# Optimization experiments

Hardware: AMD Instinct MI355X
Metric: run time of the kernel (lower is better)

The kernel has to match this reference:

```python
import jax, jax.numpy as jnp
import numpy as np

N_NODES = 100000
N_EDGES = 1600000
IN_DIM = 128
HID = 128


def setup_inputs() -> dict:
    key = jax.random.key(0)
    ks = jax.random.split(key, 8)
    x = jax.random.normal(ks[0], (N_NODES, IN_DIM), dtype=jnp.float32)
    edge_index = jax.random.randint(ks[1], (2, N_EDGES), 0, N_NODES, dtype=jnp.int32)
    s = 1.0 / np.sqrt(IN_DIM)
    # layer 1: in_dim -> hidden; layer 2: hidden -> hidden
    Wl1 = jax.random.uniform(ks[2], (IN_DIM, HID), jnp.float32, -s, s)
    bl1 = jnp.zeros((HID,), jnp.float32)
    Wr1 = jax.random.uniform(ks[3], (IN_DIM, HID), jnp.float32, -s, s)
    s2 = 1.0 / np.sqrt(HID)
    Wl2 = jax.random.uniform(ks[4], (HID, HID), jnp.float32, -s2, s2)
    bl2 = jnp.zeros((HID,), jnp.float32)
    Wr2 = jax.random.uniform(ks[5], (HID, HID), jnp.float32, -s2, s2)
    return {"x": x, "edge_index": edge_index, "Wl1": Wl1, "bl1": bl1, "Wr1": Wr1,
            "Wl2": Wl2, "bl2": bl2, "Wr2": Wr2}


def _sage_conv(h, src, dst, Wl, bl, Wr, n_nodes):
    # mean aggregation of neighbor (source) features at destination nodes
    msg = h[src]                                               # [E, D] gather
    agg = jax.ops.segment_sum(msg, dst, num_segments=n_nodes)  # [N, D]
    deg = jax.ops.segment_sum(jnp.ones((src.shape[0],), h.dtype), dst,
                              num_segments=n_nodes)            # [N]
    agg = agg / jnp.maximum(deg, 1.0)[:, None]
    # PyG SAGEConv: lin_l(aggregated) + lin_r(root); lin_r has no bias
    return agg @ Wl + bl + h @ Wr


def reference(x, edge_index, Wl1, bl1, Wr1, Wl2, bl2, Wr2):
    src, dst = edge_index[0], edge_index[1]
    n = x.shape[0]
    h = jax.nn.relu(_sage_conv(x, src, dst, Wl1, bl1, Wr1, n))
    # dropout is identity in eval mode
    h = jax.nn.relu(_sage_conv(h, src, dst, Wl2, bl2, Wr2, n))
    return h
```

## Files before the change

### kernel.cpp

```cpp
#include <hip/hip_runtime.h>
#include <stdint.h>

#define DIM 128

typedef __attribute__((ext_vector_type(8))) short short8;
typedef __attribute__((ext_vector_type(4))) float floatx4;

__device__ __forceinline__ unsigned short f2bf(float f){
  union { float f; unsigned int i; } c; c.f = f;
  unsigned int u = c.i;
  return (unsigned short)((u + 0x7fffu + ((u >> 16) & 1u)) >> 16);
}
__device__ __forceinline__ float up_lo(unsigned int v){ return __uint_as_float(v << 16); }
__device__ __forceinline__ float up_hi(unsigned int v){ return __uint_as_float(v & 0xffff0000u); }


__global__ __launch_bounds__(256) void k_cast(const float* __restrict__ in,
    unsigned short* __restrict__ out, int n4){
  int i = blockIdx.x * 256 + threadIdx.x;
  int stride = gridDim.x * 256;
  for (; i < n4; i += stride){
    float4 v = ((const float4*)in)[i];
    ushort4 o;
    o.x = f2bf(v.x); o.y = f2bf(v.y); o.z = f2bf(v.z); o.w = f2bf(v.w);
    ((ushort4*)out)[i] = o;
  }
}


__global__ __launch_bounds__(256) void k_hist256(const int* __restrict__ dst, int E,
    int* __restrict__ bktCnt){
  __shared__ int h[256];
  h[threadIdx.x] = 0;
  __syncthreads();
  int i = blockIdx.x * 256 + threadIdx.x;
  int stride = gridDim.x * 256;
  for (; i < E; i += stride) atomicAdd(&h[dst[i] >> 9], 1);
  __syncthreads();
  int v = h[threadIdx.x];
  if (v) atomicAdd(&bktCnt[threadIdx.x], v);
}

__global__ __launch_bounds__(256) void k_scanB(const int* __restrict__ bktCnt,
    int* __restrict__ bktBase, int NB){
  __shared__ int sd[256];
  int t = threadIdx.x;
  int v = (t < NB) ? bktCnt[t] : 0;
  sd[t] = v;
  __syncthreads();
  #pragma unroll
  for (int off = 1; off < 256; off <<= 1){
    int x = (t >= off) ? sd[t - off] : 0;
    __syncthreads();
    sd[t] += x;
    __syncthreads();
  }
  bktBase[t] = sd[t] - v;
}


__global__ __launch_bounds__(256) void k_hist(const int* __restrict__ dst, int E,
                                              int* __restrict__ deg){
  int e = blockIdx.x * 256 + threadIdx.x;
  if (e < E) atomicAdd(&deg[dst[e]], 1);
}

__global__ __launch_bounds__(256) void k_scan1(const int* __restrict__ deg, int N,
    int* __restrict__ out, int* __restrict__ bsum){
  __shared__ int sd[256];
  int t = threadIdx.x;
  int base = blockIdx.x * 1024 + t * 4;
  int v0=0, v1=0, v2=0, v3=0;
  if (base + 3 < N) { int4 q = *(const int4*)(deg + base); v0=q.x; v1=q.y; v2=q.z; v3=q.w; }
  else {
    if (base + 0 < N) v0 = deg[base + 0];
    if (base + 1 < N) v1 = deg[base + 1];
    if (base + 2 < N) v2 = deg[base + 2];
  }
  int s = v0 + v1 + v2 + v3;
  sd[t] = s;
  __syncthreads();
  #pragma unroll
  for (int off = 1; off < 256; off <<= 1){
    int x = (t >= off) ? sd[t - off] : 0;
    __syncthreads();
    sd[t] += x;
    __syncthreads();
  }
  int inc = sd[t];
  int exc = inc - s;
  if (base + 0 < N) out[base + 0] = exc;
  if (base + 1 < N) out[base + 1] = exc + v0;
  if (base + 2 < N) out[base + 2] = exc + v0 + v1;
  if (base + 3 < N) out[base + 3] = exc + v0 + v1 + v2;
  if (t == 255) bsum[blockIdx.x] = inc;
}

__global__ __launch_bounds__(128) void k_scan2(int* __restrict__ bsum, int nb){
  __shared__ int sd[128];
  int t = threadIdx.x;
  int v = (t < nb) ? bsum[t] : 0;
  sd[t] = v;
  __syncthreads();
  #pragma unroll
  for (int off = 1; off < 128; off <<= 1){
    int x = (t >= off) ? sd[t - off] : 0;
    __syncthreads();
    sd[t] += x;
    __syncthreads();
  }
  if (t < nb) bsum[t] = sd[t] - v;
}

__global__ __launch_bounds__(256) void k_scan3(int* __restrict__ rowptr,
    const int* __restrict__ bsum, int N, int E, int* __restrict__ cursor){
  int i = blockIdx.x * 256 + threadIdx.x;
  if (i < N){
    int v = rowptr[i] + bsum[i >> 10];
    rowptr[i] = v;
    cursor[i] = v;
  }
  if (i == 0) rowptr[N] = E;
}

__global__ __launch_bounds__(256) void k_fill(const int* __restrict__ src,
    const int* __restrict__ dst, int E, int* __restrict__ cursor, int* __restrict__ col){
  int e = blockIdx.x * 256 + threadIdx.x;
  if (e < E){
    int d = dst[e];
    int pos = atomicAdd(&cursor[d], 1);
    col[pos] = src[e];
  }
}


__global__ __launch_bounds__(256) void k_bin(const int* __restrict__ src,
    const int* __restrict__ dst, int E,
    const int* __restrict__ bucketBase, int* __restrict__ cursor,
    int2* __restrict__ binned, int NB){
  __shared__ int2 buf[4096];
  __shared__ unsigned char bidArr[4096];
  __shared__ int cnt[256], startA[256], gstart[256], gbase[256];
  int t = threadIdx.x;
  cnt[t] = 0;
  if (t < NB) gbase[t] = bucketBase[t];
  __syncthreads();
  int base = blockIdx.x * 4096;
  int s_[16], d_[16], r_[16];
  #pragma unroll
  for (int i = 0; i < 16; ++i){
    int e = base + i * 256 + t;
    bool v = (e < E);
    s_[i] = v ? src[e] : 0;
    d_[i] = v ? dst[e] : -1;
    r_[i] = v ? atomicAdd(&cnt[d_[i] >> 9], 1) : 0;
  }
  __syncthreads();
  int v = cnt[t];
  startA[t] = v;
  __syncthreads();
  #pragma unroll
  for (int off = 1; off < 256; off <<= 1){
    int y = (t >= off) ? startA[t - off] : 0;
    __syncthreads();
    startA[t] += y;
    __syncthreads();
  }
  int incl = startA[t];
  __syncthreads();
  startA[t] = incl - v;
  __syncthreads();
  #pragma unroll
  for (int i = 0; i < 16; ++i){
    if (d_[i] >= 0){
      int b = d_[i] >> 9;
      int slot = startA[b] + r_[i];
      buf[slot] = make_int2(s_[i], d_[i]);
      bidArr[slot] = (unsigned char)b;
    }
  }
  if (cnt[t] > 0) gstart[t] = atomicAdd(&cursor[t], cnt[t]);
  __syncthreads();
  int total = startA[255] + cnt[255];
  for (int j = t; j < total; j += 256){
    int b = bidArr[j];
    binned[gbase[b] + gstart[b] + (j - startA[b])] = buf[j];
  }
}


__global__ __launch_bounds__(256) void k_csr2(const int2* __restrict__ binned,
    const int* __restrict__ bktBase, int N, int* __restrict__ rowptr,
    int* __restrict__ col){
  __shared__ int cnt[512], excl[512], cur[512];
  __shared__ int sd[256];
  int b = blockIdx.x;
  int node0 = b << 9;
  int nNodes = min(512, N - node0);
  int t = threadIdx.x;
  cnt[t] = 0; cnt[t + 256] = 0;
  __syncthreads();
  int lo = bktBase[b], hi = bktBase[b + 1];
  for (int e = lo + t; e < hi; e += 256)
    atomicAdd(&cnt[binned[e].y - node0], 1);
  __syncthreads();
  int c0 = cnt[2 * t], c1 = cnt[2 * t + 1];
  int ps = c0 + c1;
  sd[t] = ps;
  __syncthreads();
  #pragma unroll
  for (int off = 1; off < 256; off <<= 1){
    int x = (t >= off) ? sd[t - off] : 0;
    __syncthreads();
    sd[t] += x;
    __syncthreads();
  }
  int pexcl = sd[t] - ps;
  excl[2 * t] = pexcl;
  excl[2 * t + 1] = pexcl + c0;
  cur[2 * t] = 0; cur[2 * t + 1] = 0;
  __syncthreads();
  for (int j = t; j < nNodes; j += 256) rowptr[node0 + j] = lo + excl[j];
  if (t == 0) rowptr[node0 + nNodes] = hi;
  for (int e = lo + t; e < hi; e += 256){
    int2 pr = binned[e];
    int dl = pr.y - node0;
    int loc = atomicAdd(&cur[dl], 1);
    col[lo + excl[dl] + loc] = pr.x;
  }
}


__device__ __forceinline__ void acc8(float* a, uint4 u){
  a[0] += up_lo(u.x); a[1] += up_hi(u.x);
  a[2] += up_lo(u.y); a[3] += up_hi(u.y);
  a[4] += up_lo(u.z); a[5] += up_hi(u.z);
  a[6] += up_lo(u.w); a[7] += up_hi(u.w);
}

__global__ __launch_bounds__(256) void k_agg_bf(const unsigned short* __restrict__ feat,
    const int* __restrict__ rowptr, const int* __restrict__ col,
    unsigned short* __restrict__ out, int N){
  int wid = (blockIdx.x * 256 + threadIdx.x) >> 6;
  if (wid >= N) return;
  int lane = threadIdx.x & 63;
  int q = lane >> 4, s = lane & 15;
  int beg = rowptr[wid], end = rowptr[wid + 1];
  int deg = end - beg;
  float a[8];
  #pragma unroll
  for (int i = 0; i < 8; ++i) a[i] = 0.f;

  int myIdx = (beg + lane < end) ? col[beg + lane] : 0;

  int o0 = q, o1 = 4 + q, o2 = 8 + q, o3 = 12 + q;
  int n0 = __shfl(myIdx, o0, 64);
  int n1 = __shfl(myIdx, o1, 64);
  int n2 = __shfl(myIdx, o2, 64);
  int n3 = __shfl(myIdx, o3, 64);
  uint4 u0 = ((const uint4*)(feat + (size_t)n0 * DIM))[s];
  uint4 u1 = ((const uint4*)(feat + (size_t)n1 * DIM))[s];
  uint4 u2 = ((const uint4*)(feat + (size_t)n2 * DIM))[s];
  uint4 u3 = ((const uint4*)(feat + (size_t)n3 * DIM))[s];

  bool g1 = deg > 16;
  int o4 = 16 + q, o5 = 20 + q, o6 = 24 + q, o7 = 28 + q;
  uint4 u4, u5, u6, u7;
  if (g1){
    int n4 = __shfl(myIdx, o4, 64);
    int n5 = __shfl(myIdx, o5, 64);
    int n6 = __shfl(myIdx, o6, 64);
    int n7 = __shfl(myIdx, o7, 64);
    u4 = ((const uint4*)(feat + (size_t)n4 * DIM))[s];
    u5 = ((const uint4*)(feat + (size_t)n5 * DIM))[s];
    u6 = ((const uint4*)(feat + (size_t)n6 * DIM))[s];
    u7 = ((const uint4*)(feat + (size_t)n7 * DIM))[s];
  }

  if (o0 < deg) acc8(a, u0);
  if (o1 < deg) acc8(a, u1);
  if (o2 < deg) acc8(a, u2);
  if (o3 < deg) acc8(a, u3);
  if (g1){
    if (o4 < deg) acc8(a, u4);
    if (o5 < deg) acc8(a, u5);
    if (o6 < deg) acc8(a, u6);
    if (o7 < deg) acc8(a, u7);
  }

  for (int e = beg + 32; e < end; e += 16){
    int i0 = e + q, i1 = e + 4 + q, i2 = e + 8 + q, i3 = e + 12 + q;
    int m0 = col[i0 < end ? i0 : beg];
    int m1 = col[i1 < end ? i1 : beg];
    int m2 = col[i2 < end ? i2 : beg];
    int m3 = col[i3 < end ? i3 : beg];
    uint4 v0 = ((const uint4*)(feat + (size_t)m0 * DIM))[s];
    uint4 v1 = ((const uint4*)(feat + (size_t)m1 * DIM))[s];
    uint4 v2 = ((const uint4*)(feat + (size_t)m2 * DIM))[s];
    uint4 v3 = ((const uint4*)(feat + (size_t)m3 * DIM))[s];
    if (i0 < end) acc8(a, v0);
    if (i1 < end) acc8(a, v1);
    if (i2 < end) acc8(a, v2);
    if (i3 < end) acc8(a, v3);
  }

  #pragma unroll
  for (int i = 0; i < 8; ++i){
    a[i] += __shfl_xor(a[i], 16, 64);
    a[i] += __shfl_xor(a[i], 32, 64);
  }
  if (q == 0){
    int d = deg;
    float r = 1.0f / (float)(d > 1 ? d : 1);
    uint4 o;
    o.x = (unsigned int)f2bf(a[0] * r) | ((unsigned int)f2bf(a[1] * r) << 16);
    o.y = (unsigned int)f2bf(a[2] * r) | ((unsigned int)f2bf(a[3] * r) << 16);
    o.z = (unsigned int)f2bf(a[4] * r) | ((unsigned int)f2bf(a[5] * r) << 16);
    o.w = (unsigned int)f2bf(a[6] * r) | ((unsigned int)f2bf(a[7] * r) << 16);
    ((uint4*)(out + (size_t)wid * DIM))[s] = o;
  }
}


__global__ __launch_bounds__(256) void k_agg_f32(const float* __restrict__ feat,
    const int* __restrict__ rowptr, const int* __restrict__ col,
    unsigned short* __restrict__ out, int N){
  int wid = (blockIdx.x * 256 + threadIdx.x) >> 6;
  if (wid >= N) return;
  int lane = threadIdx.x & 63;
  int beg = rowptr[wid], end = rowptr[wid + 1];
  float a0 = 0.f, a1 = 0.f;
  int off = lane * 2;
  int e = beg;
  for (; e + 4 <= end; e += 4){
    int s0 = col[e], s1 = col[e+1], s2 = col[e+2], s3 = col[e+3];
    float2 v0 = *(const float2*)(feat + (size_t)s0 * DIM + off);
    float2 v1 = *(const float2*)(feat + (size_t)s1 * DIM + off);
    float2 v2 = *(const float2*)(feat + (size_t)s2 * DIM + off);
    float2 v3 = *(const float2*)(feat + (size_t)s3 * DIM + off);
    a0 += v0.x + v1.x + v2.x + v3.x;
    a1 += v0.y + v1.y + v2.y + v3.y;
  }
  for (; e < end; ++e){
    float2 v = *(const float2*)(feat + (size_t)col[e] * DIM + off);
    a0 += v.x; a1 += v.y;
  }
  int d = end - beg;
  float r = 1.0f / (float)(d > 1 ? d : 1);
  a0 *= r; a1 *= r;
  unsigned int o = (unsigned int)f2bf(a0) | ((unsigned int)f2bf(a1) << 16);
  *(unsigned int*)(out + (size_t)wid * DIM + off) = o;
}


template<bool OUTBF>
__global__ __launch_bounds__(256) void k_gemm_r(const unsigned short* __restrict__ A1,
    const unsigned short* __restrict__ A2,
    const float* __restrict__ Wl, const float* __restrict__ Wr,
    const float* __restrict__ bias,
    float* __restrict__ outf, unsigned short* __restrict__ outb, int M)
{
  int lane = threadIdx.x & 63;
  int c = lane & 15, quad = lane >> 4;
  int gwid = blockIdx.x * 4 + (threadIdx.x >> 6);
  int nwaves = gridDim.x * 4;
  int half = gwid & 1;
  int colbase = half * 64;

  short8 B[2][4][4];
  #pragma unroll
  for (int w = 0; w < 2; ++w){
    const float* W = w ? Wr : Wl;
    #pragma unroll
    for (int km = 0; km < 4; ++km){
      #pragma unroll
      for (int j = 0; j < 4; ++j){
        union { short8 v; unsigned short u[8]; } tb;
        #pragma unroll
        for (int i = 0; i < 8; ++i)
          tb.u[i] = f2bf(W[(km * 32 + quad * 8 + i) * 128 + colbase + j * 16 + c]);
        B[w][km][j] = tb.v;
      }
    }
  }
  float bv[4];
  #pragma unroll
  for (int j = 0; j < 4; ++j) bv[j] = bias[colbase + j * 16 + c];

  int ntasks = M >> 4;
  for (int task = gwid >> 1; task < ntasks; task += nwaves >> 1){
    int row0 = task << 4;
    const unsigned short* ap1 = A1 + (size_t)(row0 + c) * DIM + quad * 8;
    const unsigned short* ap2 = A2 + (size_t)(row0 + c) * DIM + quad * 8;
    short8 a1[4], a2[4];
    #pragma unroll
    for (int km = 0; km < 4; ++km){
      a1[km] = *(const short8*)(ap1 + km * 32);
      a2[km] = *(const short8*)(ap2 + km * 32);
    }
    floatx4 acc[4];
    #pragma unroll
    for (int j = 0; j < 4; ++j) acc[j] = (floatx4){0.f, 0.f, 0.f, 0.f};
    #pragma unroll
    for (int km = 0; km < 4; ++km){
      #pragma unroll
      for (int j = 0; j < 4; ++j){
        acc[j] = __builtin_amdgcn_mfma_f32_16x16x32_bf16(a1[km], B[0][km][j], acc[j], 0, 0, 0);
        acc[j] = __builtin_amdgcn_mfma_f32_16x16x32_bf16(a2[km], B[1][km][j], acc[j], 0, 0, 0);
      }
    }
    #pragma unroll
    for (int j = 0; j < 4; ++j){
      int colIdx = colbase + j * 16 + c;
      #pragma unroll
      for (int r = 0; r < 4; ++r){
        int row = row0 + quad * 4 + r;
        float v = fmaxf(acc[j][r] + bv[j], 0.f);
        if (OUTBF) outb[(size_t)row * DIM + colIdx] = f2bf(v);
        else       outf[(size_t)row * DIM + colIdx] = v;
      }
    }
  }
}


__global__ __launch_bounds__(256) void k_gemm_f(const unsigned short* __restrict__ A1,
    const float* __restrict__ A2f,
    const float* __restrict__ Wl, const float* __restrict__ Wr,
    const float* __restrict__ bias, float* __restrict__ outf, int M)
{
  __shared__ unsigned short lds[2 * 128 * 128];
  for (int h = threadIdx.x; h < 128 * 128; h += 256){
    int k = h >> 7, n = h & 127;
    int idx = n * 128 + ((((k >> 3) ^ (n & 7)) << 3)) + (k & 7);
    lds[idx]         = f2bf(Wl[h]);
    lds[16384 + idx] = f2bf(Wr[h]);
  }
  __syncthreads();
  int lane = threadIdx.x & 63;
  int c = lane & 15, quad = lane >> 4;
  int gwid = blockIdx.x * 4 + (threadIdx.x >> 6);
  int nwaves = gridDim.x * 4;
  int ntasks = M >> 4;
  for (int task = gwid; task < ntasks; task += nwaves){
    int row0 = task << 4;
    floatx4 acc[8];
    #pragma unroll
    for (int j = 0; j < 8; ++j) acc[j] = (floatx4){0.f, 0.f, 0.f, 0.f};
    const unsigned short* ap1 = A1 + (size_t)(row0 + c) * DIM + quad * 8;
    #pragma unroll
    for (int km = 0; km < 4; ++km){
      short8 a = *(const short8*)(ap1 + km * 32);
      int kb = (km << 2) + quad;
      #pragma unroll
      for (int j = 0; j < 8; ++j){
        short8 b = *(const short8*)(&lds[(j * 16 + c) * 128 + ((kb ^ (c & 7)) << 3)]);
        acc[j] = __builtin_amdgcn_mfma_f32_16x16x32_bf16(a, b, acc[j], 0, 0, 0);
      }
    }
    #pragma unroll
    for (int km = 0; km < 4; ++km){
      const float* ap2 = A2f + (size_t)(row0 + c) * DIM + quad * 8;
      float4 p0 = *(const float4*)(ap2 + km * 32);
      float4 p1 = *(const float4*)(ap2 + km * 32 + 4);
      union { short8 v; unsigned short u[8]; } ua;
      ua.u[0] = f2bf(p0.x); ua.u[1] = f2bf(p0.y);
      ua.u[2] = f2bf(p0.z); ua.u[3] = f2bf(p0.w);
      ua.u[4] = f2bf(p1.x); ua.u[5] = f2bf(p1.y);
      ua.u[6] = f2bf(p1.z); ua.u[7] = f2bf(p1.w);
      int kb = (km << 2) + quad;
      #pragma unroll
      for (int j = 0; j < 8; ++j){
        short8 b = *(const short8*)(&lds[16384 + (j * 16 + c) * 128 + ((kb ^ (c & 7)) << 3)]);
        acc[j] = __builtin_amdgcn_mfma_f32_16x16x32_bf16(ua.v, b, acc[j], 0, 0, 0);
      }
    }
    #pragma unroll
    for (int j = 0; j < 8; ++j){
      int colIdx = j * 16 + c;
      float bvv = bias[colIdx];
      #pragma unroll
      for (int r = 0; r < 4; ++r){
        int row = row0 + quad * 4 + r;
        outf[(size_t)row * DIM + colIdx] = fmaxf(acc[j][r] + bvv, 0.f);
      }
    }
  }
}


extern "C" void kernel_launch(void* const* d_in, const int* in_sizes, int n_in,
                              void* d_out, int out_size, void* d_ws, size_t ws_size,
                              hipStream_t stream)
{
  const float* x   = (const float*)d_in[0];
  const int*   ei  = (const int*)d_in[1];
  const float* Wl1 = (const float*)d_in[2];
  const float* bl1 = (const float*)d_in[3];
  const float* Wr1 = (const float*)d_in[4];
  const float* Wl2 = (const float*)d_in[5];
  const float* bl2 = (const float*)d_in[6];
  const float* Wr2 = (const float*)d_in[7];

  const int N = in_sizes[0] / DIM;
  const int E = in_sizes[1] / 2;
  const int* src  = ei;
  const int* dstI = ei + E;
  const int NB = (N + 511) >> 9;

  char* p = (char*)d_ws;
  auto alloc = [&](size_t bytes) -> char* {
    char* r = p; p += (bytes + 255) & ~((size_t)255); return r;
  };
  int* rowptr   = (int*)alloc((size_t)(N + 1) * 4);
  int* deg      = (int*)alloc((size_t)N * 4);
  int* bsum     = (int*)alloc(1024);
  int* bktCnt   = (int*)alloc(1024);
  int* bktBase  = (int*)alloc(2048);
  int* bktCur   = (int*)alloc(1024);
  int* col      = (int*)alloc((size_t)E * 4);
  unsigned short* aggb = (unsigned short*)alloc((size_t)N * DIM * 2);
  unsigned short* xb   = (unsigned short*)alloc((size_t)N * DIM * 2);
  unsigned short* h1b  = (unsigned short*)alloc((size_t)N * DIM * 2);
  size_t need_big = (size_t)(p - (char*)d_ws);
  const bool big = (ws_size >= need_big) && (NB <= 255);
  int2* binned = (int2*)aggb;

  int gE = (E + 255) / 256;
  int gAgg = (N * 64 + 255) / 256;

  if (big){
    hipMemsetAsync(bktCnt, 0, 1024, stream);
    hipMemsetAsync(bktCur, 0, 1024, stream);
    k_hist256<<<1024, 256, 0, stream>>>(dstI, E, bktCnt);
    k_scanB<<<1, 256, 0, stream>>>(bktCnt, bktBase, NB);
    k_bin<<<(E + 4095) / 4096, 256, 0, stream>>>(src, dstI, E, bktBase, bktCur,
                                                 binned, NB);
    k_csr2<<<NB, 256, 0, stream>>>(binned, bktBase, N, rowptr, col);
    int n4 = N * DIM / 4;
    k_cast<<<8192, 256, 0, stream>>>(x, xb, n4);
    k_agg_bf<<<gAgg, 256, 0, stream>>>(xb, rowptr, col, aggb, N);
    k_gemm_r<true><<<512, 256, 0, stream>>>(aggb, xb, Wl1, Wr1, bl1,
                                            nullptr, h1b, N);
    k_agg_bf<<<gAgg, 256, 0, stream>>>(h1b, rowptr, col, aggb, N);
    k_gemm_r<false><<<512, 256, 0, stream>>>(aggb, h1b, Wl2, Wr2, bl2,
                                             (float*)d_out, nullptr, N);
  } else {
    hipMemsetAsync(deg, 0, (size_t)N * 4, stream);
    k_hist<<<gE, 256, 0, stream>>>(dstI, E, deg);
    int nb = (N + 1023) / 1024;
    k_scan1<<<nb, 256, 0, stream>>>(deg, N, rowptr, bsum);
    k_scan2<<<1, 128, 0, stream>>>(bsum, nb);
    k_scan3<<<(N + 255) / 256, 256, 0, stream>>>(rowptr, bsum, N, E, deg);
    k_fill<<<gE, 256, 0, stream>>>(src, dstI, E, deg, col);
    float* h1 = (float*)d_out;
    k_agg_f32<<<gAgg, 256, 0, stream>>>(x, rowptr, col, aggb, N);
    k_gemm_f<<<512, 256, 0, stream>>>(aggb, x, Wl1, Wr1, bl1, h1, N);
    k_agg_f32<<<gAgg, 256, 0, stream>>>(h1, rowptr, col, aggb, N);
    k_gemm_f<<<512, 256, 0, stream>>>(aggb, h1, Wl2, Wr2, bl2, (float*)d_out, N);
  }
}
```

Baseline: 338.4 us.

## Fuse cast with bucket histogram, prefetch GEMM tiles, widen CSR build blocks

Merges the fp32-to-bf16 cast of x with the destination bucket histogram into one kernel and merges the two memsets into one by making the counter buffers adjacent. The binning chunk shrinks to 2048 edges per block, the CSR build runs 1024 threads per bucket, and the GEMM now software-prefetches the next task's A tiles while computing the current one, with launch bounds raised for occupancy. The aim is to cut launch overhead and latency stalls. The cost is more registers from the prefetch and fewer blocks for the cast.

Measured after the change: 329.4 us. 2.7% less time.

```diff
diff --git a/kernel.cpp b/kernel.cpp
--- a/kernel.cpp
+++ b/kernel.cpp
@@ -15,27 +15,21 @@
 __device__ __forceinline__ float up_hi(unsigned int v){ return __uint_as_float(v & 0xffff0000u); }
 
 
-__global__ __launch_bounds__(256) void k_cast(const float* __restrict__ in,
-    unsigned short* __restrict__ out, int n4){
+__global__ __launch_bounds__(256) void k_prep(const float* __restrict__ in,
+    unsigned short* __restrict__ out, int n4,
+    const int* __restrict__ dst, int E, int* __restrict__ bktCnt){
+  __shared__ int h[256];
+  h[threadIdx.x] = 0;
+  __syncthreads();
   int i = blockIdx.x * 256 + threadIdx.x;
   int stride = gridDim.x * 256;
-  for (; i < n4; i += stride){
-    float4 v = ((const float4*)in)[i];
+  for (int k = i; k < n4; k += stride){
+    float4 v = ((const float4*)in)[k];
     ushort4 o;
     o.x = f2bf(v.x); o.y = f2bf(v.y); o.z = f2bf(v.z); o.w = f2bf(v.w);
-    ((ushort4*)out)[i] = o;
-  }
-}
-
-
-__global__ __launch_bounds__(256) void k_hist256(const int* __restrict__ dst, int E,
-    int* __restrict__ bktCnt){
-  __shared__ int h[256];
-  h[threadIdx.x] = 0;
-  __syncthreads();
-  int i = blockIdx.x * 256 + threadIdx.x;
-  int stride = gridDim.x * 256;
-  for (; i < E; i += stride) atomicAdd(&h[dst[i] >> 9], 1);
+    ((ushort4*)out)[k] = o;
+  }
+  for (int k = i; k < E; k += stride) atomicAdd(&h[dst[k] >> 9], 1);
   __syncthreads();
   int v = h[threadIdx.x];
   if (v) atomicAdd(&bktCnt[threadIdx.x], v);
@@ -134,21 +128,23 @@
 }
 
 
+#define BINCH 2048
+
 __global__ __launch_bounds__(256) void k_bin(const int* __restrict__ src,
     const int* __restrict__ dst, int E,
     const int* __restrict__ bucketBase, int* __restrict__ cursor,
     int2* __restrict__ binned, int NB){
-  __shared__ int2 buf[4096];
-  __shared__ unsigned char bidArr[4096];
+  __shared__ int2 buf[BINCH];
+  __shared__ unsigned char bidArr[BINCH];
   __shared__ int cnt[256], startA[256], gstart[256], gbase[256];
   int t = threadIdx.x;
   cnt[t] = 0;
   if (t < NB) gbase[t] = bucketBase[t];
   __syncthreads();
-  int base = blockIdx.x * 4096;
-  int s_[16], d_[16], r_[16];
-  #pragma unroll
-  for (int i = 0; i < 16; ++i){
+  int base = blockIdx.x * BINCH;
+  int s_[8], d_[8], r_[8];
+  #pragma unroll
+  for (int i = 0; i < 8; ++i){
     int e = base + i * 256 + t;
     bool v = (e < E);
     s_[i] = v ? src[e] : 0;
@@ -171,7 +167,7 @@
   startA[t] = incl - v;
   __syncthreads();
   #pragma unroll
-  for (int i = 0; i < 16; ++i){
+  for (int i = 0; i < 8; ++i){
     if (d_[i] >= 0){
       int b = d_[i] >> 9;
       int slot = startA[b] + r_[i];
@@ -189,7 +185,7 @@
 }
 
 
-__global__ __launch_bounds__(256) void k_csr2(const int2* __restrict__ binned,
+__global__ __launch_bounds__(1024) void k_csr2(const int2* __restrict__ binned,
     const int* __restrict__ bktBase, int N, int* __restrict__ rowptr,
     int* __restrict__ col){
   __shared__ int cnt[512], excl[512], cur[512];
@@ -198,31 +194,36 @@
   int node0 = b << 9;
   int nNodes = min(512, N - node0);
   int t = threadIdx.x;
-  cnt[t] = 0; cnt[t + 256] = 0;
+  if (t < 512){ cnt[t] = 0; cur[t] = 0; }
   __syncthreads();
   int lo = bktBase[b], hi = bktBase[b + 1];
-  for (int e = lo + t; e < hi; e += 256)
+  for (int e = lo + t; e < hi; e += 1024)
     atomicAdd(&cnt[binned[e].y - node0], 1);
   __syncthreads();
-  int c0 = cnt[2 * t], c1 = cnt[2 * t + 1];
-  int ps = c0 + c1;
-  sd[t] = ps;
+  int c0 = 0, c1 = 0, ps = 0;
+  if (t < 256){
+    c0 = cnt[2 * t]; c1 = cnt[2 * t + 1];
+    ps = c0 + c1;
+    sd[t] = ps;
+  }
   __syncthreads();
   #pragma unroll
   for (int off = 1; off < 256; off <<= 1){
-    int x = (t >= off) ? sd[t - off] : 0;
-    __syncthreads();
-    sd[t] += x;
-    __syncthreads();
-  }
-  int pexcl = sd[t] - ps;
-  excl[2 * t] = pexcl;
-  excl[2 * t + 1] = pexcl + c0;
-  cur[2 * t] = 0; cur[2 * t + 1] = 0;
-  __syncthreads();
-  for (int j = t; j < nNodes; j += 256) rowptr[node0 + j] = lo + excl[j];
+    int x = 0;
+    if (t < 256 && t >= off) x = sd[t - off];
+    __syncthreads();
+    if (t < 256) sd[t] += x;
+    __syncthreads();
+  }
+  if (t < 256){
+    int pexcl = sd[t] - ps;
+    excl[2 * t] = pexcl;
+    excl[2 * t + 1] = pexcl + c0;
+  }
+  __syncthreads();
+  for (int j = t; j < nNodes; j += 1024) rowptr[node0 + j] = lo + excl[j];
   if (t == 0) rowptr[node0 + nNodes] = hi;
-  for (int e = lo + t; e < hi; e += 256){
+  for (int e = lo + t; e < hi; e += 1024){
     int2 pr = binned[e];
     int dl = pr.y - node0;
     int loc = atomicAdd(&cur[dl], 1);
@@ -354,7 +355,7 @@
 
 
 template<bool OUTBF>
-__global__ __launch_bounds__(256) void k_gemm_r(const unsigned short* __restrict__ A1,
+__global__ __launch_bounds__(256, 2) void k_gemm_r(const unsigned short* __restrict__ A1,
     const unsigned short* __restrict__ A2,
     const float* __restrict__ Wl, const float* __restrict__ Wr,
     const float* __restrict__ bias,
@@ -388,15 +389,28 @@
   for (int j = 0; j < 4; ++j) bv[j] = bias[colbase + j * 16 + c];
 
   int ntasks = M >> 4;
-  for (int task = gwid >> 1; task < ntasks; task += nwaves >> 1){
-    int row0 = task << 4;
-    const unsigned short* ap1 = A1 + (size_t)(row0 + c) * DIM + quad * 8;
-    const unsigned short* ap2 = A2 + (size_t)(row0 + c) * DIM + quad * 8;
-    short8 a1[4], a2[4];
+  int stride = nwaves >> 1;
+  int task = gwid >> 1;
+  short8 a1[4], a2[4];
+  if (task < ntasks){
+    const unsigned short* ap1 = A1 + (size_t)((task << 4) + c) * DIM + quad * 8;
+    const unsigned short* ap2 = A2 + (size_t)((task << 4) + c) * DIM + quad * 8;
     #pragma unroll
     for (int km = 0; km < 4; ++km){
       a1[km] = *(const short8*)(ap1 + km * 32);
       a2[km] = *(const short8*)(ap2 + km * 32);
+    }
+  }
+  for (; task < ntasks; task += stride){
+    int nxt = task + stride;
+    int pt = nxt < ntasks ? nxt : task;
+    const unsigned short* p1 = A1 + (size_t)((pt << 4) + c) * DIM + quad * 8;
+    const unsigned short* p2 = A2 + (size_t)((pt << 4) + c) * DIM + quad * 8;
+    short8 n1[4], n2[4];
+    #pragma unroll
+    for (int km = 0; km < 4; ++km){
+      n1[km] = *(const short8*)(p1 + km * 32);
+      n2[km] = *(const short8*)(p2 + km * 32);
     }
     floatx4 acc[4];
     #pragma unroll
@@ -409,6 +423,7 @@
         acc[j] = __builtin_amdgcn_mfma_f32_16x16x32_bf16(a2[km], B[1][km][j], acc[j], 0, 0, 0);
       }
     }
+    int row0 = task << 4;
     #pragma unroll
     for (int j = 0; j < 4; ++j){
       int colIdx = colbase + j * 16 + c;
@@ -420,6 +435,8 @@
         else       outf[(size_t)row * DIM + colIdx] = v;
       }
     }
+    #pragma unroll
+    for (int km = 0; km < 4; ++km){ a1[km] = n1[km]; a2[km] = n2[km]; }
   }
 }
 
@@ -516,8 +533,8 @@
   int* deg      = (int*)alloc((size_t)N * 4);
   int* bsum     = (int*)alloc(1024);
   int* bktCnt   = (int*)alloc(1024);
+  int* bktCur   = (int*)alloc(1024);
   int* bktBase  = (int*)alloc(2048);
-  int* bktCur   = (int*)alloc(1024);
   int* col      = (int*)alloc((size_t)E * 4);
   unsigned short* aggb = (unsigned short*)alloc((size_t)N * DIM * 2);
   unsigned short* xb   = (unsigned short*)alloc((size_t)N * DIM * 2);
@@ -530,15 +547,13 @@
   int gAgg = (N * 64 + 255) / 256;
 
   if (big){
-    hipMemsetAsync(bktCnt, 0, 1024, stream);
-    hipMemsetAsync(bktCur, 0, 1024, stream);
-    k_hist256<<<1024, 256, 0, stream>>>(dstI, E, bktCnt);
+    int n4 = N * DIM / 4;
+    hipMemsetAsync(bktCnt, 0, 2048, stream);
+    k_prep<<<1024, 256, 0, stream>>>(x, xb, n4, dstI, E, bktCnt);
     k_scanB<<<1, 256, 0, stream>>>(bktCnt, bktBase, NB);
-    k_bin<<<(E + 4095) / 4096, 256, 0, stream>>>(src, dstI, E, bktBase, bktCur,
-                                                 binned, NB);
-    k_csr2<<<NB, 256, 0, stream>>>(binned, bktBase, N, rowptr, col);
-    int n4 = N * DIM / 4;
-    k_cast<<<8192, 256, 0, stream>>>(x, xb, n4);
+    k_bin<<<(E + BINCH - 1) / BINCH, 256, 0, stream>>>(src, dstI, E, bktBase, bktCur,
+                                                       binned, NB);
+    k_csr2<<<NB, 1024, 0, stream>>>(binned, bktBase, N, rowptr, col);
     k_agg_bf<<<gAgg, 256, 0, stream>>>(xb, rowptr, col, aggb, N);
     k_gemm_r<true><<<512, 256, 0, stream>>>(aggb, xb, Wl1, Wr1, bl1,
                                             nullptr, h1b, N);
```
